# Performance work log

Measured on AMD Instinct MI355X. Metric: run time of the kernel, lower is better.

The kernel has to match this reference:

```python
import jax, jax.numpy as jnp
import numpy as np
import math

D_MODEL = 768
H = 12
D_K = D_MODEL // H


def setup_inputs() -> dict:
    key = jax.random.key(0)
    ks = jax.random.split(key, 12)
    B, S = 2, 2048
    q = jax.random.normal(ks[0], (B, S, D_MODEL), dtype=jnp.float32)
    k = jax.random.normal(ks[1], (B, S, D_MODEL), dtype=jnp.float32)
    v = jax.random.normal(ks[2], (B, S, D_MODEL), dtype=jnp.float32)
    mask = jax.random.randint(ks[3], (1, 1, S, S), 0, 2, dtype=jnp.int32)
    scale = 1.0 / math.sqrt(D_MODEL)
    w_q = jax.random.normal(ks[4], (D_MODEL, D_MODEL), dtype=jnp.float32) * scale
    b_q = jnp.zeros((D_MODEL,), dtype=jnp.float32)
    w_k = jax.random.normal(ks[5], (D_MODEL, D_MODEL), dtype=jnp.float32) * scale
    b_k = jnp.zeros((D_MODEL,), dtype=jnp.float32)
    w_v = jax.random.normal(ks[6], (D_MODEL, D_MODEL), dtype=jnp.float32) * scale
    b_v = jnp.zeros((D_MODEL,), dtype=jnp.float32)
    w_o = jax.random.normal(ks[7], (D_MODEL, D_MODEL), dtype=jnp.float32) * scale
    b_o = jnp.zeros((D_MODEL,), dtype=jnp.float32)
    return {"q": q, "k": k, "v": v, "mask": mask,
            "w_q": w_q, "b_q": b_q, "w_k": w_k, "b_k": b_k,
            "w_v": w_v, "b_v": b_v, "w_o": w_o, "b_o": b_o}


def reference(q, k, v, mask, w_q, b_q, w_k, b_k, w_v, b_v, w_o, b_o):
    B, S, _ = q.shape
    # torch nn.Linear: y = x @ W^T + b
    qp = (q @ w_q.T + b_q).reshape(B, S, H, D_K).transpose(0, 2, 1, 3)  # [B,H,S,Dk]
    kp = (k @ w_k.T + b_k).reshape(B, S, H, D_K).transpose(0, 2, 1, 3)
    vp = (v @ w_v.T + b_v).reshape(B, S, H, D_K).transpose(0, 2, 1, 3)
    # full [B,H,S,S] score matrix (the memory-bound round-trip)
    scores = jnp.einsum('bhqd,bhkd->bhqk', qp, kp) / math.sqrt(D_K)
    scores = jnp.where(mask == 0, jnp.float32(-1e9), scores)
    attn = jax.nn.softmax(scores, axis=-1)
    x = jnp.einsum('bhqk,bhkd->bhqd', attn, vp)  # [B,H,S,Dk]
    x = x.transpose(0, 2, 1, 3).reshape(B, S, H * D_K)
    return x @ w_o.T + b_o
```

## Files before the change

### kernel.cpp

```cpp
#include <hip/hip_runtime.h>
#include <hip/hip_bf16.h>

typedef __attribute__((ext_vector_type(8))) __bf16 bf16x8;
typedef __attribute__((ext_vector_type(8))) short short8;
typedef __attribute__((ext_vector_type(4))) float f32x4;

#define LOG2E 1.44269504088896f
#define SCL (0.125f * 1.44269504088896f)

static __device__ __forceinline__ ushort f2bf(float f) {
  union { float f; unsigned u; } x; x.f = f;
  unsigned r = x.u + 0x7fffu + ((x.u >> 16) & 1u);
  return (ushort)(r >> 16);
}

static __device__ __forceinline__ unsigned cvt_pk_bf16(float a, float b) {
  unsigned r;
  asm("v_cvt_pk_bf16_f32 %0, %1, %2" : "=v"(r) : "v"(a), "v"(b));
  return r;
}

static __device__ __forceinline__ void gll16(const ushort* g, ushort* l) {
  __builtin_amdgcn_global_load_lds(
      (const __attribute__((address_space(1))) unsigned*)g,
      (__attribute__((address_space(3))) unsigned*)l, 16, 0, 0);
}

#define NQ 3145728u
#define NW 589824u
__global__ __launch_bounds__(256)
void cvt_all(const float* __restrict__ q, const float* __restrict__ k,
             const float* __restrict__ v,
             const float* __restrict__ wq, const float* __restrict__ wk,
             const float* __restrict__ wv, const float* __restrict__ wo,
             ushort* __restrict__ dst)
{
  size_t i = ((size_t)blockIdx.x * 256 + threadIdx.x) * 4;
  const float* src; size_t off;
  if (i < NQ)                { src = q;  off = i; }
  else if (i < 2u * NQ)      { src = k;  off = i - NQ; }
  else if (i < 3u * NQ)      { src = v;  off = i - 2u * NQ; }
  else {
    size_t j = i - 3u * NQ;
    if (j < NW)            { src = wq; off = j; }
    else if (j < 2u * NW)  { src = wk; off = j - NW; }
    else if (j < 3u * NW)  { src = wv; off = j - 2u * NW; }
    else                   { src = wo; off = j - 3u * NW; }
  }
  f32x4 x = *(const f32x4*)(src + off);
  uint2 o;
  o.x = cvt_pk_bf16(x[0], x[1]);
  o.y = cvt_pk_bf16(x[2], x[3]);
  *(uint2*)(dst + i) = o;
}

__global__ __launch_bounds__(256)
void mask_pack(const int* __restrict__ mask, unsigned long long* __restrict__ mb)
{
  size_t gw = (size_t)blockIdx.x * 4 + (threadIdx.x >> 6);
  int lane = threadIdx.x & 63;
  int mk = mask[gw * 64 + lane];
  unsigned long long bits = __ballot(mk != 0);
  if (lane == 0) mb[gw] = bits;
}

template<int MODE>
static __device__ __forceinline__ void gemm_core(const ushort* __restrict__ A,
                                                 const ushort* __restrict__ Wrow0,
                                                 const float* __restrict__ bias0,
                                                 void* __restrict__ outv,
                                                 int m0, int c0)
{
  constexpr int K = 768;
  constexpr int BK = 64;
  __shared__ ushort As[2][128 * BK];
  __shared__ ushort Bs[2][128 * BK];
  const int tid  = threadIdx.x;
  const int lane = tid & 63;
  const int wid  = tid >> 6;
  const int wr = (wid >> 1) * 64;
  const int wc = (wid & 1) * 64;

  f32x4 acc[4][4];
#pragma unroll
  for (int i = 0; i < 4; i++)
#pragma unroll
    for (int j = 0; j < 4; j++) acc[i][j] = f32x4{0.f, 0.f, 0.f, 0.f};

  const ushort* gA[4]; const ushort* gB[4];
  int loff[4];
#pragma unroll
  for (int s = 0; s < 4; s++) {
    int idx = tid + s * 256;
    int row = idx >> 3, col = (idx & 7) * 8;
    gA[s] = A     + (size_t)(m0 + row) * K + col;
    gB[s] = Wrow0 + (size_t)row * K + col;
    loff[s] = idx * 8;
  }

  const int fr  = lane & 15;
  const int kg8 = (lane >> 4) * 8;

#pragma unroll
  for (int s = 0; s < 4; s++) {
    gll16(gA[s], &As[0][loff[s]]);
    gll16(gB[s], &Bs[0][loff[s]]);
  }
  __syncthreads();

  int cur = 0;
  for (int t = 0; t < K / BK; t++) {
    if (t < K / BK - 1) {
      const int kt = (t + 1) * BK;
#pragma unroll
      for (int s = 0; s < 4; s++) {
        gll16(gA[s] + kt, &As[cur ^ 1][loff[s]]);
        gll16(gB[s] + kt, &Bs[cur ^ 1][loff[s]]);
      }
    }
    bf16x8 af[2][4], wf[2][4];
#pragma unroll
    for (int kk = 0; kk < 2; kk++) {
#pragma unroll
      for (int i = 0; i < 4; i++) af[kk][i] = *(const bf16x8*)&As[cur][(wr + i * 16 + fr) * BK + kk * 32 + kg8];
#pragma unroll
      for (int j = 0; j < 4; j++) wf[kk][j] = *(const bf16x8*)&Bs[cur][(wc + j * 16 + fr) * BK + kk * 32 + kg8];
    }
#pragma unroll
    for (int kk = 0; kk < 2; kk++)
#pragma unroll
      for (int i = 0; i < 4; i++)
#pragma unroll
        for (int j = 0; j < 4; j++)
          acc[i][j] = __builtin_amdgcn_mfma_f32_16x16x32_bf16(af[kk][i], wf[kk][j], acc[i][j], 0, 0, 0);
    __syncthreads();
    cur ^= 1;
  }

#pragma unroll
  for (int i = 0; i < 4; i++) {
#pragma unroll
    for (int j = 0; j < 4; j++) {
#pragma unroll
      for (int r = 0; r < 4; r++) {
        int m  = m0 + wr + i * 16 + (lane >> 4) * 4 + r;
        int lc = wc + j * 16 + fr;
        float val = acc[i][j][r] + bias0[lc];
        if (MODE == 0) {
          int nn = c0 + lc;
          int hh = nn >> 6, dk = nn & 63;
          ((ushort*)outv)[(((size_t)(m >> 11) * 12 + hh) * 2048 + (m & 2047)) * 64 + dk] = f2bf(val);
        } else {
          ((float*)outv)[(size_t)m * 768 + c0 + lc] = val;
        }
      }
    }
  }
}

__global__ __launch_bounds__(256)
void qkv_gemm2(const ushort* __restrict__ CV,
               const float* __restrict__ bq, const float* __restrict__ bk,
               const float* __restrict__ bv,
               ushort* __restrict__ Qp, ushort* __restrict__ Kp, ushort* __restrict__ Vp)
{
  const int m0 = blockIdx.x * 128;
  const int n0 = blockIdx.y * 128;
  const int proj = n0 / 768;
  const int c0 = n0 - proj * 768;
  const ushort* A  = CV + (size_t)proj * NQ;
  const ushort* Wc = CV + (size_t)3 * NQ;
  const float* bias = (proj == 0) ? bq : (proj == 1) ? bk : bv;
  ushort* O = (proj == 0) ? Qp : (proj == 1) ? Kp : Vp;
  gemm_core<0>(A, Wc + (size_t)n0 * 768, bias + c0, O, m0, c0);
}

__global__ __launch_bounds__(256)
void o_gemm2(const ushort* __restrict__ X, const ushort* __restrict__ Wo,
             const float* __restrict__ bo, float* __restrict__ out)
{
  const int m0 = blockIdx.x * 128;
  const int n0 = blockIdx.y * 128;
  gemm_core<1>(X, Wo + (size_t)n0 * 768, bo + n0, out, m0, n0);
}

__global__ __launch_bounds__(256, 3)
void attn_kernel(const ushort* __restrict__ Qp, const ushort* __restrict__ Kp,
                 const ushort* __restrict__ Vp,
                 const unsigned long long* __restrict__ mb,
                 ushort* __restrict__ X)
{
  constexpr int S = 2048;
  __shared__ ushort Ks[128][64];
  __shared__ ushort Vt[64][136];
  __shared__ ushort Ps[4][16][128];

  const int tid  = threadIdx.x;
  const int lane = tid & 63;
  const int w    = tid >> 6;
  const int bid  = blockIdx.x;
  const int bh = (bid & 7) + 8 * (bid >> 8);
  const int qb = (bid >> 3) & 31;
  const int b = bh / 12, h = bh % 12;

  const ushort* Qb = Qp + (size_t)bh * S * 64;
  const ushort* Kb = Kp + (size_t)bh * S * 64;
  const ushort* Vb = Vp + (size_t)bh * S * 64;

  const int q0  = qb * 64;
  const int fr  = lane & 15;
  const int g   = lane >> 4;
  const int g4  = g * 4;
  const int kg8 = g * 8;
  const int qrow4 = q0 + w * 16 + g4;

  const int qrow = q0 + w * 16 + fr;
  bf16x8 qf0 = *(const bf16x8*)&Qb[(size_t)qrow * 64 + kg8];
  bf16x8 qf1 = *(const bf16x8*)&Qb[(size_t)qrow * 64 + 32 + kg8];

  float m_s = -1e9f;
  float l_s = 0.f;
  f32x4 accO[4];
#pragma unroll
  for (int ni = 0; ni < 4; ni++) accO[ni] = f32x4{0.f, 0.f, 0.f, 0.f};

  const int skey = tid >> 2;
  const int sc0  = (tid & 3) * 16;
  const int kxor = (skey & 7) << 3;
  const uint4* mb4 = (const uint4*)mb;

  short8 kr0, kr1, kr2, kr3, vr0, vr1, vr2, vr3;
  {
    const ushort* kb = Kb + (size_t)skey * 64 + sc0;
    const ushort* vb = Vb + (size_t)skey * 64 + sc0;
    kr0 = *(const short8*)kb;          kr1 = *(const short8*)(kb + 8);
    kr2 = *(const short8*)(kb + 4096); kr3 = *(const short8*)(kb + 4104);
    vr0 = *(const short8*)vb;          vr1 = *(const short8*)(vb + 8);
    vr2 = *(const short8*)(vb + 4096); vr3 = *(const short8*)(vb + 4104);
  }

  for (int tt = 0; tt < 16; tt++) {
    __syncthreads();
    *(short8*)&Ks[skey][sc0 ^ kxor]            = kr0;
    *(short8*)&Ks[skey][(sc0 + 8) ^ kxor]      = kr1;
    *(short8*)&Ks[64 + skey][sc0 ^ kxor]       = kr2;
    *(short8*)&Ks[64 + skey][(sc0 + 8) ^ kxor] = kr3;
#pragma unroll
    for (int i = 0; i < 8; i++) {
      Vt[sc0 + i][skey]          = (ushort)vr0[i];
      Vt[sc0 + 8 + i][skey]      = (ushort)vr1[i];
      Vt[sc0 + i][64 + skey]     = (ushort)vr2[i];
      Vt[sc0 + 8 + i][64 + skey] = (ushort)vr3[i];
    }
    __syncthreads();

    uint4 mq = mb4[(size_t)qrow * 16 + tt];
    unsigned mw[4] = {mq.x, mq.y, mq.z, mq.w};

    if (tt < 15) {
      const ushort* kb = Kb + (size_t)((tt + 1) * 128 + skey) * 64 + sc0;
      const ushort* vb = Vb + (size_t)((tt + 1) * 128 + skey) * 64 + sc0;
      kr0 = *(const short8*)kb;          kr1 = *(const short8*)(kb + 8);
      kr2 = *(const short8*)(kb + 4096); kr3 = *(const short8*)(kb + 4104);
      vr0 = *(const short8*)vb;          vr1 = *(const short8*)(vb + 8);
      vr2 = *(const short8*)(vb + 4096); vr3 = *(const short8*)(vb + 4104);
    }

    f32x4 sc8[8];
#pragma unroll
    for (int ni = 0; ni < 8; ni++) {
      const int row = ni * 16 + fr;
      const int rx = (row & 7) << 3;
      bf16x8 kf0 = *(const bf16x8*)&Ks[row][kg8 ^ rx];
      bf16x8 kf1 = *(const bf16x8*)&Ks[row][(32 + kg8) ^ rx];
      f32x4 c = {0.f, 0.f, 0.f, 0.f};
      c = __builtin_amdgcn_mfma_f32_16x16x32_bf16(kf0, qf0, c, 0, 0, 0);
      c = __builtin_amdgcn_mfma_f32_16x16x32_bf16(kf1, qf1, c, 0, 0, 0);
      sc8[ni] = c;
    }

    float p[32];
#pragma unroll
    for (int ni = 0; ni < 8; ni++)
#pragma unroll
      for (int r = 0; r < 4; r++) p[ni * 4 + r] = sc8[ni][r] * SCL;

    float t16[16];
#pragma unroll
    for (int z = 0; z < 16; z++) t16[z] = fmaxf(p[z], p[z + 16]);
#pragma unroll
    for (int z = 0; z < 8; z++) t16[z] = fmaxf(t16[z], t16[z + 8]);
#pragma unroll
    for (int z = 0; z < 4; z++) t16[z] = fmaxf(t16[z], t16[z + 4]);
    float mx = fmaxf(fmaxf(t16[0], t16[1]), fmaxf(t16[2], t16[3]));
    mx = fmaxf(mx, __shfl_xor(mx, 16));
    mx = fmaxf(mx, __shfl_xor(mx, 32));

    bool need = mx > m_s + 11.5f;
    if (__any(need)) {
      float mn = need ? mx : m_s;
      float al = exp2f(m_s - mn);
      m_s = mn;
      l_s *= al;
#pragma unroll
      for (int r = 0; r < 4; r++) {
        float alr = __shfl(al, g4 + r);
#pragma unroll
        for (int ni = 0; ni < 4; ni++) accO[ni][r] *= alr;
      }
    }
    const float mr = m_s;

#pragma unroll
    for (int ni = 0; ni < 8; ni++) {
      unsigned wv = mw[ni >> 1] >> (((ni & 1) * 16) + g4);
#pragma unroll
      for (int r = 0; r < 4; r++) {
        float t = exp2f(p[ni * 4 + r] - mr);
        p[ni * 4 + r] = ((wv >> r) & 1u) ? t : 0.f;
      }
    }

#pragma unroll
    for (int z = 0; z < 16; z++) t16[z] = p[z] + p[z + 16];
#pragma unroll
    for (int z = 0; z < 8; z++) t16[z] += t16[z + 8];
#pragma unroll
    for (int z = 0; z < 4; z++) t16[z] += t16[z + 4];
    float ls = (t16[0] + t16[1]) + (t16[2] + t16[3]);
    ls += __shfl_xor(ls, 16);
    ls += __shfl_xor(ls, 32);
    l_s += ls;

    const int px = (fr & 7) << 3;
#pragma unroll
    for (int ni = 0; ni < 8; ni++) {
      uint2 pk;
      pk.x = cvt_pk_bf16(p[ni * 4 + 0], p[ni * 4 + 1]);
      pk.y = cvt_pk_bf16(p[ni * 4 + 2], p[ni * 4 + 3]);
      *(uint2*)&Ps[w][fr][(ni * 16 + g4) ^ px] = pk;
    }

#pragma unroll
    for (int ks = 0; ks < 4; ks++) {
      bf16x8 pf = *(const bf16x8*)&Ps[w][fr][(ks * 32 + kg8) ^ px];
#pragma unroll
      for (int ni = 0; ni < 4; ni++) {
        bf16x8 vf = *(const bf16x8*)&Vt[ni * 16 + fr][ks * 32 + kg8];
        accO[ni] = __builtin_amdgcn_mfma_f32_16x16x32_bf16(pf, vf, accO[ni], 0, 0, 0);
      }
    }
  }

  float inv[4];
#pragma unroll
  for (int r = 0; r < 4; r++) inv[r] = 1.f / __shfl(l_s, g4 + r);
#pragma unroll
  for (int ni = 0; ni < 4; ni++) {
#pragma unroll
    for (int r = 0; r < 4; r++) {
      int qq = qrow4 + r;
      float o = accO[ni][r] * inv[r];
      X[((size_t)b * S + qq) * 768 + h * 64 + ni * 16 + fr] = f2bf(o);
    }
  }
}

extern "C" void kernel_launch(void* const* d_in, const int* in_sizes, int n_in,
                              void* d_out, int out_size, void* d_ws, size_t ws_size,
                              hipStream_t stream) {
  const float* q  = (const float*)d_in[0];
  const float* k  = (const float*)d_in[1];
  const float* v  = (const float*)d_in[2];
  const int* mask = (const int*)d_in[3];
  const float* wq = (const float*)d_in[4];
  const float* bq = (const float*)d_in[5];
  const float* wk = (const float*)d_in[6];
  const float* bk = (const float*)d_in[7];
  const float* wv = (const float*)d_in[8];
  const float* bv = (const float*)d_in[9];
  const float* wo = (const float*)d_in[10];
  const float* bo = (const float*)d_in[11];
  float* out = (float*)d_out;

  ushort* CV = (ushort*)d_ws;
  ushort* Qp = CV + (size_t)3 * NQ + (size_t)4 * NW;
  ushort* Kp = Qp + NQ;
  ushort* Vp = Kp + NQ;
  ushort* Xb = Vp + NQ;
  unsigned long long* mbuf = (unsigned long long*)CV;

  cvt_all<<<11520, 256, 0, stream>>>(q, k, v, wq, wk, wv, wo, CV);
  qkv_gemm2<<<dim3(32, 18), dim3(256), 0, stream>>>(CV, bq, bk, bv, Qp, Kp, Vp);
  mask_pack<<<16384, 256, 0, stream>>>(mask, mbuf);
  attn_kernel<<<768, 256, 0, stream>>>(Qp, Kp, Vp, mbuf, Xb);
  o_gemm2<<<dim3(32, 6), dim3(256), 0, stream>>>(Xb, CV + (size_t)3 * NQ + (size_t)3 * NW, bo, out);
}
```

Before: 244.6 us.

## Fuse mask packing into convert kernel and skew V transpose layout in LDS

Folds the mask bit-packing kernel into the fp32-to-bf16 conversion launch as extra blocks, which removes one kernel launch. The packed mask now lives after the Xb buffer instead of aliasing the converted inputs, because the two writes now happen in the same launch. The transposed V tile in LDS gets a row-dependent column rotation on write and the matching rotation on read. This is meant to cut bank conflicts from the scalar transpose stores, at the cost of slightly more index arithmetic.

```diff
diff --git a/kernel.cpp b/kernel.cpp
--- a/kernel.cpp
+++ b/kernel.cpp
@@ -28,14 +28,25 @@
 
 #define NQ 3145728u
 #define NW 589824u
+#define CVT_BLOCKS 11520
 __global__ __launch_bounds__(256)
-void cvt_all(const float* __restrict__ q, const float* __restrict__ k,
-             const float* __restrict__ v,
-             const float* __restrict__ wq, const float* __restrict__ wk,
-             const float* __restrict__ wv, const float* __restrict__ wo,
-             ushort* __restrict__ dst)
+void cvt_mask(const float* __restrict__ q, const float* __restrict__ k,
+              const float* __restrict__ v,
+              const float* __restrict__ wq, const float* __restrict__ wk,
+              const float* __restrict__ wv, const float* __restrict__ wo,
+              ushort* __restrict__ dst,
+              const int* __restrict__ mask, unsigned long long* __restrict__ mb)
 {
-  size_t i = ((size_t)blockIdx.x * 256 + threadIdx.x) * 4;
+  const int bid = blockIdx.x;
+  if (bid >= CVT_BLOCKS) {
+    size_t gw = (size_t)(bid - CVT_BLOCKS) * 4 + (threadIdx.x >> 6);
+    int lane = threadIdx.x & 63;
+    int mk = mask[gw * 64 + lane];
+    unsigned long long bits = __ballot(mk != 0);
+    if (lane == 0) mb[gw] = bits;
+    return;
+  }
+  size_t i = ((size_t)bid * 256 + threadIdx.x) * 4;
   const float* src; size_t off;
   if (i < NQ)                { src = q;  off = i; }
   else if (i < 2u * NQ)      { src = k;  off = i - NQ; }
@@ -52,16 +63,6 @@
   o.x = cvt_pk_bf16(x[0], x[1]);
   o.y = cvt_pk_bf16(x[2], x[3]);
   *(uint2*)(dst + i) = o;
-}
-
-__global__ __launch_bounds__(256)
-void mask_pack(const int* __restrict__ mask, unsigned long long* __restrict__ mb)
-{
-  size_t gw = (size_t)blockIdx.x * 4 + (threadIdx.x >> 6);
-  int lane = threadIdx.x & 63;
-  int mk = mask[gw * 64 + lane];
-  unsigned long long bits = __ballot(mk != 0);
-  if (lane == 0) mb[gw] = bits;
 }
 
 template<int MODE>
@@ -227,6 +228,8 @@
   const int skey = tid >> 2;
   const int sc0  = (tid & 3) * 16;
   const int kxor = (skey & 7) << 3;
+  const int vc0 = (skey + sc0) & 127;
+  const int vc1 = (64 + skey + sc0) & 127;
   const uint4* mb4 = (const uint4*)mb;
 
   short8 kr0, kr1, kr2, kr3, vr0, vr1, vr2, vr3;
@@ -247,10 +250,10 @@
     *(short8*)&Ks[64 + skey][(sc0 + 8) ^ kxor] = kr3;
 #pragma unroll
     for (int i = 0; i < 8; i++) {
-      Vt[sc0 + i][skey]          = (ushort)vr0[i];
-      Vt[sc0 + 8 + i][skey]      = (ushort)vr1[i];
-      Vt[sc0 + i][64 + skey]     = (ushort)vr2[i];
-      Vt[sc0 + 8 + i][64 + skey] = (ushort)vr3[i];
+      Vt[sc0 + i][vc0]     = (ushort)vr0[i];
+      Vt[sc0 + 8 + i][vc0] = (ushort)vr1[i];
+      Vt[sc0 + i][vc1]     = (ushort)vr2[i];
+      Vt[sc0 + 8 + i][vc1] = (ushort)vr3[i];
     }
     __syncthreads();
 
@@ -346,7 +349,7 @@
       bf16x8 pf = *(const bf16x8*)&Ps[w][fr][(ks * 32 + kg8) ^ px];
 #pragma unroll
       for (int ni = 0; ni < 4; ni++) {
-        bf16x8 vf = *(const bf16x8*)&Vt[ni * 16 + fr][ks * 32 + kg8];
+        bf16x8 vf = *(const bf16x8*)&Vt[ni * 16 + fr][(ks * 32 + kg8 + ni * 16) & 127];
         accO[ni] = __builtin_amdgcn_mfma_f32_16x16x32_bf16(pf, vf, accO[ni], 0, 0, 0);
       }
     }
@@ -388,11 +391,10 @@
   ushort* Kp = Qp + NQ;
   ushort* Vp = Kp + NQ;
   ushort* Xb = Vp + NQ;
-  unsigned long long* mbuf = (unsigned long long*)CV;
-
-  cvt_all<<<11520, 256, 0, stream>>>(q, k, v, wq, wk, wv, wo, CV);
+  unsigned long long* mbuf = (unsigned long long*)(Xb + NQ);
+
+  cvt_mask<<<27904, 256, 0, stream>>>(q, k, v, wq, wk, wv, wo, CV, mask, mbuf);
   qkv_gemm2<<<dim3(32, 18), dim3(256), 0, stream>>>(CV, bq, bk, bv, Qp, Kp, Vp);
-  mask_pack<<<16384, 256, 0, stream>>>(mask, mbuf);
   attn_kernel<<<768, 256, 0, stream>>>(Qp, Kp, Vp, mbuf, Xb);
   o_gemm2<<<dim3(32, 6), dim3(256), 0, stream>>>(Xb, CV + (size_t)3 * NQ + (size_t)3 * NW, bo, out);
 }
```

Result: faster. 233.8 us (-4.4%).
